# Kernel tuning notes

Measured on AMD Instinct MI355X. Metric: run time of the kernel, lower is better.

The kernel has to match this reference:

```python
import jax, jax.numpy as jnp
import numpy as np

DIM = 512; NH = 8; AG = 144; WIN = 18; PS = 12; B = 128; N0 = 320


def _pool_matrix(in_size, out_size):
    # PyTorch AdaptiveAvgPool2d window rule: start=floor(i*in/out), end=ceil((i+1)*in/out)
    P = np.zeros((out_size, in_size), np.float32)
    for i in range(out_size):
        s = (i * in_size) // out_size
        e = -((-(i + 1) * in_size) // out_size)
        P[i, s:e] = 1.0 / (e - s)
    return jnp.asarray(P)


def setup_inputs() -> dict:
    key = jax.random.key(0)
    ks = jax.random.split(key, 12)
    std = 0.02
    return {
        "x": jax.random.normal(ks[0], (B, N0, DIM), jnp.float32),
        "qkv_w": jax.random.normal(ks[1], (DIM, 3 * DIM), jnp.float32) * 0.02,
        "proj_w": jax.random.normal(ks[2], (DIM, DIM), jnp.float32) * 0.02,
        "proj_b": jnp.zeros((DIM,), jnp.float32),
        "dwc_w": jax.random.normal(ks[3], (DIM, 1, 3, 3), jnp.float32) * 0.1,
        "dwc_b": jnp.zeros((DIM,), jnp.float32),
        "an_bias": jax.random.normal(ks[4], (NH, AG, 7, 7), jnp.float32) * std,
        "na_bias": jax.random.normal(ks[5], (NH, AG, 7, 7), jnp.float32) * std,
        "ah_bias": jax.random.normal(ks[6], (1, NH, AG, WIN, 1), jnp.float32) * std,
        "aw_bias": jax.random.normal(ks[7], (1, NH, AG, 1, WIN), jnp.float32) * std,
        "ha_bias": jax.random.normal(ks[8], (1, NH, WIN, 1, AG), jnp.float32) * std,
        "wa_bias": jax.random.normal(ks[9], (1, NH, 1, WIN, AG), jnp.float32) * std,
    }


def reference(x, qkv_w, proj_w, proj_b, dwc_w, dwc_b,
              an_bias, na_bias, ah_bias, aw_bias, ha_bias, wa_bias):
    b, n0, c = x.shape
    x1 = jnp.pad(x, ((0, 0), (2, 2), (0, 0)))          # pad 2 tokens each side
    n = n0 + 4
    h = w = int(n ** 0.5)
    hd = c // NH
    scale = hd ** -0.5

    qkv = x1 @ qkv_w                                    # (b, n, 3c), no bias
    q, k, v = jnp.split(qkv, 3, axis=-1)

    # agent tokens: adaptive avg pool of q on the (h, w) grid to (PS, PS)
    P = _pool_matrix(h, PS)                             # (12, 18)
    qg = q.reshape(b, h, w, c)
    agent = jnp.einsum('oh,bhwc,pw->bopc', P, qg, P).reshape(b, AG, c)

    def heads(t):
        return t.reshape(b, n, NH, hd).transpose(0, 2, 1, 3)
    q, k, v = heads(q), heads(k), heads(v)              # (b, H, n, hd)
    ag = agent.reshape(b, AG, NH, hd).transpose(0, 2, 1, 3)  # (b, H, A, hd)

    # stage 1: agent <- keys  (ac_bias is concatenated then sliced off => no-op)
    pb1 = jax.image.resize(an_bias, (NH, AG, WIN, WIN), 'bilinear').reshape(1, NH, AG, WIN * WIN)
    pb2 = (ah_bias + aw_bias).reshape(1, NH, AG, WIN * WIN)
    agent_attn = jax.nn.softmax(
        jnp.einsum('bhad,bhnd->bhan', ag * scale, k) + pb1 + pb2, axis=-1)
    agent_v = jnp.einsum('bhan,bhnd->bhad', agent_attn, v)   # (b, H, A, hd)

    # stage 2: queries <- agents (ca_bias sliced off => no-op)
    ab1 = jax.image.resize(na_bias, (NH, AG, WIN, WIN), 'bilinear') \
        .reshape(1, NH, AG, WIN * WIN).transpose(0, 1, 3, 2)  # (1, H, n, A)
    ab2 = (ha_bias + wa_bias).reshape(1, NH, WIN * WIN, AG)
    q_attn = jax.nn.softmax(
        jnp.einsum('bhnd,bhad->bhna', q * scale, ag) + ab1 + ab2, axis=-1)
    out = jnp.einsum('bhna,bhad->bhnd', q_attn, agent_v)
    out = out.transpose(0, 2, 1, 3).reshape(b, n, c)

    # depthwise conv skip on v
    vimg = v.transpose(0, 2, 1, 3).reshape(b, h, w, c).transpose(0, 3, 1, 2)  # (b, c, h, w)
    dwc = jax.lax.conv_general_dilated(vimg, dwc_w, (1, 1), 'SAME',
                                       feature_group_count=c)
    dwc = dwc + dwc_b[None, :, None, None]
    out = out + dwc.transpose(0, 2, 3, 1).reshape(b, n, c)

    out = out @ proj_w + proj_b
    return out[:, 2:-2, :]
```

## Files before the change

kernel.cpp:

```cpp
#include <hip/hip_runtime.h>

typedef unsigned short u16;
typedef short bf16x8 __attribute__((ext_vector_type(8)));
typedef float f32x4 __attribute__((ext_vector_type(4)));

#define B_    128
#define N0_   320
#define C_    512
#define NH_   8
#define HD_   64
#define NTOK  324
#define H_    18
#define AG_   144
#define SCALE 0.125f

typedef __attribute__((address_space(3))) unsigned int as3_u32;
typedef __attribute__((address_space(1))) const unsigned int as1_u32;

__device__ __forceinline__ void gl_lds16(const void* g, void* l) {
  __builtin_amdgcn_global_load_lds((as1_u32*)(unsigned long long)g,
                                   (as3_u32*)(unsigned int)(unsigned long long)l,
                                   16, 0, 0);
}

__device__ __forceinline__ float bfu2f(u16 u) {
  union { unsigned int u; float f; } v; v.u = ((unsigned int)u) << 16; return v.f;
}
__device__ __forceinline__ u16 f2bfu(float f) {
  union { float f; unsigned int u; } v; v.f = f;
  unsigned int r = v.u + 0x7fffu + ((v.u >> 16) & 1u);
  return (u16)(r >> 16);
}

__global__ __launch_bounds__(256) void conv_x(const float* __restrict__ x, u16* __restrict__ xp)
{
  const int idx = blockIdx.x * 256 + threadIdx.x;
  const int row = idx >> 6, c8 = idx & 63;
  const int b = row / NTOK, t = row - b * NTOK;
  u16 o[8];
  if (t < 2 || t >= 322) {
    #pragma unroll
    for (int j = 0; j < 8; ++j) o[j] = 0;
  } else {
    const float* src = x + ((size_t)(b * N0_ + (t - 2))) * C_ + c8 * 8;
    const float4 f0 = *(const float4*)(src);
    const float4 f1 = *(const float4*)(src + 4);
    o[0]=f2bfu(f0.x); o[1]=f2bfu(f0.y); o[2]=f2bfu(f0.z); o[3]=f2bfu(f0.w);
    o[4]=f2bfu(f1.x); o[5]=f2bfu(f1.y); o[6]=f2bfu(f1.z); o[7]=f2bfu(f1.w);
  }
  *(bf16x8*)&xp[(size_t)row * C_ + c8 * 8] = *(bf16x8*)o;
}

__global__ __launch_bounds__(256) void tconv(const float* __restrict__ W, u16* __restrict__ Wt, int ncols)
{
  __shared__ float T[64][65];
  const int k0 = blockIdx.x * 64, n0 = blockIdx.y * 64;
  const int tid = threadIdx.x;
  const int rr = tid >> 4, cc = tid & 15;
  #pragma unroll
  for (int i = 0; i < 4; ++i) {
    const float4 f = *(const float4*)&W[(size_t)(k0 + i * 16 + rr) * ncols + n0 + cc * 4];
    T[i * 16 + rr][cc * 4 + 0] = f.x; T[i * 16 + rr][cc * 4 + 1] = f.y;
    T[i * 16 + rr][cc * 4 + 2] = f.z; T[i * 16 + rr][cc * 4 + 3] = f.w;
  }
  __syncthreads();
  #pragma unroll
  for (int i = 0; i < 4; ++i) {
    const int n = i * 16 + rr;
    ushort4 u;
    u.x = f2bfu(T[cc * 4 + 0][n]); u.y = f2bfu(T[cc * 4 + 1][n]);
    u.z = f2bfu(T[cc * 4 + 2][n]); u.w = f2bfu(T[cc * 4 + 3][n]);
    *(ushort4*)&Wt[(size_t)(n0 + n) * 512 + k0 + cc * 4] = u;
  }
}

template<int MODE>
__global__ __launch_bounds__(256) void mfma_gemm(
    const u16* __restrict__ A, const u16* __restrict__ Bt,
    u16* __restrict__ qb, u16* __restrict__ kb, u16* __restrict__ vb,
    const float* __restrict__ bias, float* __restrict__ outf)
{
  __shared__ __align__(16) u16 As[128 * 64];
  __shared__ __align__(16) u16 Bs[128 * 64];
  const int bx = blockIdx.x;
  const int by = blockIdx.y;
  const int tid = threadIdx.x;
  const int wv = tid >> 6, lane = tid & 63;
  const int lr = lane & 15, lk = lane >> 4;
  const int wr = wv >> 1, wc = wv & 1;
  const int si = lane >> 3, slot = lane & 7;

  size_t arow_src[4];
  #pragma unroll
  for (int jj = 0; jj < 4; ++jj) {
    const int rl = (wv * 4 + jj) * 8 + si;
    const int r = by * 128 + rl;
    if (MODE == 0) {
      arow_src[jj] = (size_t)r;
    } else {
      const int b2 = r / N0_, ii = r - b2 * N0_;
      arow_src[jj] = (size_t)b2 * NTOK + ii + 2;
    }
  }

  f32x4 acc[4][4] = {};
  for (int k0 = 0; k0 < 512; k0 += 64) {
    __syncthreads();
    #pragma unroll
    for (int jj = 0; jj < 4; ++jj) {
      const int rl = (wv * 4 + jj) * 8 + si;
      const int c = slot ^ (rl & 7);
      gl_lds16(A + arow_src[jj] * 512 + k0 + c * 8,
               (char*)As + (wv * 4 + jj) * 1024);
      gl_lds16(Bt + (size_t)(bx * 128 + rl) * 512 + k0 + c * 8,
               (char*)Bs + (wv * 4 + jj) * 1024);
    }
    __syncthreads();
    #pragma unroll
    for (int kk = 0; kk < 2; ++kk) {
      bf16x8 af[4], bf[4];
      #pragma unroll
      for (int m = 0; m < 4; ++m) {
        const int row = wr * 64 + m * 16 + lr;
        af[m] = *(const bf16x8*)((const char*)As + row * 128 + (((kk * 4 + lk) ^ (row & 7)) << 4));
      }
      #pragma unroll
      for (int n = 0; n < 4; ++n) {
        const int row = wc * 64 + n * 16 + lr;
        bf[n] = *(const bf16x8*)((const char*)Bs + row * 128 + (((kk * 4 + lk) ^ (row & 7)) << 4));
      }
      #pragma unroll
      for (int m = 0; m < 4; ++m)
        #pragma unroll
        for (int n = 0; n < 4; ++n)
          acc[m][n] = __builtin_amdgcn_mfma_f32_16x16x32_bf16(af[m], bf[n], acc[m][n], 0, 0, 0);
    }
  }

  if (MODE == 0) {
    const int mat = (bx * 128) >> 9;
    u16* outp = (mat == 0) ? qb : (mat == 1) ? kb : vb;
    #pragma unroll
    for (int m = 0; m < 4; ++m) {
      #pragma unroll
      for (int r = 0; r < 4; ++r) {
        const int row = by * 128 + wr * 64 + m * 16 + lk * 4 + r;
        const int b = row / NTOK, t = row - b * NTOK;
        #pragma unroll
        for (int n = 0; n < 4; ++n) {
          const int col = bx * 128 + wc * 64 + n * 16 + lr;
          const int rem = col & 511, h = rem >> 6, d = rem & 63;
          outp[(((size_t)(b * NH_ + h)) * NTOK + t) * HD_ + d] = f2bfu(acc[m][n][r]);
        }
      }
    }
  } else {
    #pragma unroll
    for (int m = 0; m < 4; ++m) {
      #pragma unroll
      for (int r = 0; r < 4; ++r) {
        const int row = by * 128 + wr * 64 + m * 16 + lk * 4 + r;
        #pragma unroll
        for (int n = 0; n < 4; ++n) {
          const int col = bx * 128 + wc * 64 + n * 16 + lr;
          outf[(size_t)row * C_ + col] = acc[m][n][r] + bias[col];
        }
      }
    }
  }
}

__global__ void bias_kernel(const float* __restrict__ an, const float* __restrict__ na,
                            const float* __restrict__ ah, const float* __restrict__ aw,
                            const float* __restrict__ ha, const float* __restrict__ wa,
                            float* __restrict__ bAN, float* __restrict__ bNA)
{
  const int blk = blockIdx.x;
  const int h = blk / AG_, a = blk - h * AG_;
  const int tid = threadIdx.x;
  if (tid >= NTOK) return;
  const int y = tid / H_, x = tid - y * H_;
  float cy = (y + 0.5f) * (7.0f / 18.0f) - 0.5f; cy = fminf(fmaxf(cy, 0.f), 6.f);
  float cx = (x + 0.5f) * (7.0f / 18.0f) - 0.5f; cx = fminf(fmaxf(cx, 0.f), 6.f);
  const int y0 = (int)floorf(cy); const float ty = cy - y0; const int y1 = min(y0 + 1, 6);
  const int x0 = (int)floorf(cx); const float tx = cx - x0; const int x1 = min(x0 + 1, 6);
  const float w00 = (1.f - ty) * (1.f - tx), w01 = (1.f - ty) * tx;
  const float w10 = ty * (1.f - tx), w11 = ty * tx;
  const float* anp = an + (size_t)blk * 49;
  const float* nap = na + (size_t)blk * 49;
  const float van = w00 * anp[y0*7+x0] + w01 * anp[y0*7+x1] + w10 * anp[y1*7+x0] + w11 * anp[y1*7+x1];
  const float vna = w00 * nap[y0*7+x0] + w01 * nap[y0*7+x1] + w10 * nap[y1*7+x0] + w11 * nap[y1*7+x1];
  bAN[(size_t)blk * NTOK + tid] = van + ah[(size_t)blk * H_ + y] + aw[(size_t)blk * H_ + x];
  bNA[((size_t)h * NTOK + tid) * AG_ + a] =
      vna + ha[((size_t)h * H_ + y) * AG_ + a] + wa[((size_t)h * H_ + x) * AG_ + a];
}

__global__ __launch_bounds__(512) void pool_kernel(const u16* __restrict__ qb, u16* __restrict__ agb)
{
  const int blk = blockIdx.x;
  const int b = blk / AG_, a = blk - b * AG_;
  const int o = a / 12, pc = a - o * 12;
  const int y0 = (3 * o) >> 1, x0 = (3 * pc) >> 1;
  const int c = threadIdx.x; const int h = c >> 6, d = c & 63;
  const size_t base = ((size_t)(b * NH_ + h)) * NTOK * HD_ + d;
  const int t00 = (y0 * H_ + x0) * HD_;
  const float v = bfu2f(qb[base + t00]) + bfu2f(qb[base + t00 + HD_])
                + bfu2f(qb[base + t00 + H_ * HD_]) + bfu2f(qb[base + t00 + H_ * HD_ + HD_]);
  agb[((size_t)(b * NH_ + h)) * AG_ * HD_ + a * HD_ + d] = f2bfu(0.25f * v);
}

__global__ __launch_bounds__(512) void dwc_kernel(
    const u16* __restrict__ vb, const float* __restrict__ dwc_w,
    const float* __restrict__ dwc_b, u16* __restrict__ aob)
{
  __shared__ __align__(16) u16 vL[NTOK * 64];
  const int bh = blockIdx.x, b = bh >> 3, h = bh & 7;
  const int tid = threadIdx.x;
  const bf16x8* vs = (const bf16x8*)(vb + (size_t)bh * NTOK * HD_);
  for (int idx = tid; idx < NTOK * 8; idx += 512)
    ((bf16x8*)vL)[idx] = vs[idx];
  const int d = tid & 63, tg = tid >> 6;
  float w9[9];
  #pragma unroll
  for (int j = 0; j < 9; ++j) w9[j] = dwc_w[(size_t)(h * 64 + d) * 9 + j];
  const float cb = dwc_b[h * 64 + d];
  __syncthreads();
  for (int t = tg; t < NTOK; t += 8) {
    const int y = t / H_, x = t - y * H_;
    float conv = cb;
    #pragma unroll
    for (int ky = 0; ky < 3; ++ky) {
      const int yy = y + ky - 1;
      if (yy < 0 || yy >= H_) continue;
      #pragma unroll
      for (int kx = 0; kx < 3; ++kx) {
        const int xc = x + kx - 1;
        if (xc < 0 || xc >= H_) continue;
        conv += w9[ky * 3 + kx] * bfu2f(vL[(yy * H_ + xc) * 64 + d]);
      }
    }
    aob[((size_t)b * NTOK + t) * C_ + h * 64 + d] = f2bfu(conv);
  }
}

__global__ __launch_bounds__(576) void stage1_v2(
    const u16* __restrict__ kb, const u16* __restrict__ vb,
    const u16* __restrict__ agb, const float* __restrict__ bAN,
    u16* __restrict__ avbT)
{
  __shared__ __align__(16) u16 vT[64 * 360];
  __shared__ __align__(16) u16 pW[9][16][40];
  const int bh = blockIdx.x, h = bh & 7;
  const int tid = threadIdx.x;

  for (int idx = tid; idx < 64 * 16; idx += 576)
    avbT[((size_t)bh * 64 + (idx >> 4)) * 160 + 144 + (idx & 15)] = 0;

  const u16* vsrc = vb + (size_t)bh * NTOK * HD_;
  for (int idx = tid; idx < 64 * 352; idx += 576) {
    const int d = idx & 63, n = idx >> 6;
    vT[d * 360 + n] = (n < NTOK) ? vsrc[n * HD_ + d] : (u16)0;
  }
  __syncthreads();

  const int mt = tid >> 6;
  const int l  = tid & 63, lr = l & 15, lk = l >> 4;

  const u16* aga = agb + ((size_t)bh * AG_ + mt * 16 + lr) * HD_ + lk * 8;
  const bf16x8 a0 = *(const bf16x8*)(aga);
  const bf16x8 a1 = *(const bf16x8*)(aga + 32);

  f32x4 acc[21];
  const u16* kbase = kb + (size_t)bh * NTOK * HD_ + lk * 8;
  #pragma unroll
  for (int nt = 0; nt < 21; ++nt) {
    const bf16x8 b0 = *(const bf16x8*)(kbase + (size_t)(nt * 16 + lr) * HD_);
    const bf16x8 b1 = *(const bf16x8*)(kbase + (size_t)(nt * 16 + lr) * HD_ + 32);
    f32x4 c = {0.f, 0.f, 0.f, 0.f};
    c = __builtin_amdgcn_mfma_f32_16x16x32_bf16(a0, b0, c, 0, 0, 0);
    c = __builtin_amdgcn_mfma_f32_16x16x32_bf16(a1, b1, c, 0, 0, 0);
    acc[nt] = c;
  }

  const float* bb = bAN + ((size_t)h * AG_ + mt * 16) * NTOK;
  float mx[4] = {-1e30f, -1e30f, -1e30f, -1e30f};
  #pragma unroll
  for (int nt = 0; nt < 21; ++nt) {
    const int col = nt * 16 + lr;
    const bool valid = (nt < 20) || (lr < 4);
    #pragma unroll
    for (int r = 0; r < 4; ++r) {
      float s = -1e30f;
      if (valid) s = acc[nt][r] * SCALE + bb[(lk * 4 + r) * NTOK + col];
      acc[nt][r] = s;
      mx[r] = fmaxf(mx[r], s);
    }
  }
  #pragma unroll
  for (int r = 0; r < 4; ++r) {
    #pragma unroll
    for (int o = 1; o < 16; o <<= 1) mx[r] = fmaxf(mx[r], __shfl_xor(mx[r], o));
  }
  float sm[4] = {0.f, 0.f, 0.f, 0.f};
  #pragma unroll
  for (int nt = 0; nt < 21; ++nt) {
    #pragma unroll
    for (int r = 0; r < 4; ++r) {
      const float e = __expf(acc[nt][r] - mx[r]);
      acc[nt][r] = e;
      sm[r] += e;
    }
  }
  #pragma unroll
  for (int r = 0; r < 4; ++r) {
    #pragma unroll
    for (int o = 1; o < 16; o <<= 1) sm[r] += __shfl_xor(sm[r], o);
    sm[r] = 1.0f / sm[r];
  }

  f32x4 ov[4];
  #pragma unroll
  for (int nt2 = 0; nt2 < 4; ++nt2) ov[nt2] = (f32x4){0.f, 0.f, 0.f, 0.f};
  for (int ks = 0; ks < 11; ++ks) {
    #pragma unroll
    for (int half = 0; half < 2; ++half) {
      const int nt = 2 * ks + half;
      #pragma unroll
      for (int r = 0; r < 4; ++r)
        pW[mt][lk * 4 + r][half * 16 + lr] = (nt < 21) ? f2bfu(acc[nt][r] * sm[r]) : (u16)0;
    }
    const bf16x8 pa = *(const bf16x8*)&pW[mt][lr][lk * 8];
    #pragma unroll
    for (int nt2 = 0; nt2 < 4; ++nt2) {
      const bf16x8 vf = *(const bf16x8*)&vT[(nt2 * 16 + lr) * 360 + ks * 32 + lk * 8];
      ov[nt2] = __builtin_amdgcn_mfma_f32_16x16x32_bf16(pa, vf, ov[nt2], 0, 0, 0);
    }
  }
  #pragma unroll
  for (int nt2 = 0; nt2 < 4; ++nt2) {
    #pragma unroll
    for (int r = 0; r < 4; ++r)
      avbT[((size_t)bh * 64 + nt2 * 16 + lr) * 160 + mt * 16 + lk * 4 + r] = f2bfu(ov[nt2][r]);
  }
}

__global__ __launch_bounds__(512) void stage2_v2(
    const u16* __restrict__ qb, const u16* __restrict__ agb,
    const u16* __restrict__ avbT, const float* __restrict__ bNA,
    u16* __restrict__ aob)
{
  __shared__ __align__(16) u16 pW[8][16][40];
  const int bh = blockIdx.x, b = bh >> 3, h = bh & 7;
  const int tid = threadIdx.x;
  const int wv = tid >> 6, l = tid & 63, lr = l & 15, lk = l >> 4;

  for (int mt = wv; mt < 21; mt += 8) {
    const int arow = min(mt * 16 + lr, NTOK - 1);
    const u16* qa = qb + ((size_t)bh * NTOK + arow) * HD_ + lk * 8;
    const bf16x8 a0 = *(const bf16x8*)(qa);
    const bf16x8 a1 = *(const bf16x8*)(qa + 32);

    f32x4 acc[9];
    #pragma unroll
    for (int nt = 0; nt < 9; ++nt) {
      const u16* bp = agb + ((size_t)bh * AG_ + nt * 16 + lr) * HD_ + lk * 8;
      f32x4 c = {0.f, 0.f, 0.f, 0.f};
      c = __builtin_amdgcn_mfma_f32_16x16x32_bf16(a0, *(const bf16x8*)(bp), c, 0, 0, 0);
      c = __builtin_amdgcn_mfma_f32_16x16x32_bf16(a1, *(const bf16x8*)(bp + 32), c, 0, 0, 0);
      acc[nt] = c;
    }

    float mx[4] = {-1e30f, -1e30f, -1e30f, -1e30f};
    #pragma unroll
    for (int nt = 0; nt < 9; ++nt) {
      #pragma unroll
      for (int r = 0; r < 4; ++r) {
        const int trow = min(mt * 16 + lk * 4 + r, NTOK - 1);
        const float s = acc[nt][r] * SCALE + bNA[((size_t)h * NTOK + trow) * AG_ + nt * 16 + lr];
        acc[nt][r] = s;
        mx[r] = fmaxf(mx[r], s);
      }
    }
    #pragma unroll
    for (int r = 0; r < 4; ++r) {
      #pragma unroll
      for (int o = 1; o < 16; o <<= 1) mx[r] = fmaxf(mx[r], __shfl_xor(mx[r], o));
    }
    float sm[4] = {0.f, 0.f, 0.f, 0.f};
    #pragma unroll
    for (int nt = 0; nt < 9; ++nt) {
      #pragma unroll
      for (int r = 0; r < 4; ++r) {
        const float e = __expf(acc[nt][r] - mx[r]);
        acc[nt][r] = e;
        sm[r] += e;
      }
    }
    #pragma unroll
    for (int r = 0; r < 4; ++r) {
      #pragma unroll
      for (int o = 1; o < 16; o <<= 1) sm[r] += __shfl_xor(sm[r], o);
      sm[r] = 1.0f / sm[r];
    }

    f32x4 ov[4];
    #pragma unroll
    for (int nt2 = 0; nt2 < 4; ++nt2) ov[nt2] = (f32x4){0.f, 0.f, 0.f, 0.f};
    const u16* avbase = avbT + (size_t)bh * 64 * 160;
    for (int ks = 0; ks < 5; ++ks) {
      #pragma unroll
      for (int half = 0; half < 2; ++half) {
        const int nt = 2 * ks + half;
        #pragma unroll
        for (int r = 0; r < 4; ++r)
          pW[wv][lk * 4 + r][half * 16 + lr] = (nt < 9) ? f2bfu(acc[nt][r] * sm[r]) : (u16)0;
      }
      const bf16x8 pa = *(const bf16x8*)&pW[wv][lr][lk * 8];
      #pragma unroll
      for (int nt2 = 0; nt2 < 4; ++nt2) {
        const bf16x8 vf = *(const bf16x8*)(avbase + (size_t)(nt2 * 16 + lr) * 160 + ks * 32 + lk * 8);
        ov[nt2] = __builtin_amdgcn_mfma_f32_16x16x32_bf16(pa, vf, ov[nt2], 0, 0, 0);
      }
    }

    #pragma unroll
    for (int nt2 = 0; nt2 < 4; ++nt2) {
      #pragma unroll
      for (int r = 0; r < 4; ++r) {
        const int t = mt * 16 + lk * 4 + r;
        if (t < NTOK) {
          const size_t o = ((size_t)b * NTOK + t) * C_ + h * 64 + nt2 * 16 + lr;
          aob[o] = f2bfu(bfu2f(aob[o]) + ov[nt2][r]);
        }
      }
    }
  }
}

extern "C" void kernel_launch(void* const* d_in, const int* in_sizes, int n_in,
                              void* d_out, int out_size, void* d_ws, size_t ws_size,
                              hipStream_t stream)
{
  (void)in_sizes; (void)n_in; (void)out_size;
  const float* x      = (const float*)d_in[0];
  const float* qkv_w  = (const float*)d_in[1];
  const float* proj_w = (const float*)d_in[2];
  const float* proj_b = (const float*)d_in[3];
  const float* dwc_w  = (const float*)d_in[4];
  const float* dwc_b  = (const float*)d_in[5];
  const float* an     = (const float*)d_in[6];
  const float* na     = (const float*)d_in[7];
  const float* ah     = (const float*)d_in[8];
  const float* aw     = (const float*)d_in[9];
  const float* ha     = (const float*)d_in[10];
  const float* wa     = (const float*)d_in[11];

  char* ws = (char*)d_ws;
  const size_t QB   = (size_t)B_ * NH_ * NTOK * HD_ * 2;
  const size_t AGB  = (size_t)B_ * NH_ * AG_  * HD_ * 2;
  const size_t AVTB = (size_t)B_ * NH_ * 64 * 160 * 2;
  const size_t BB   = (size_t)NH_ * AG_ * NTOK * 4;
  const size_t WQ   = (size_t)1536 * 512 * 2;
  const size_t WP   = (size_t)512 * 512 * 2;
  u16* qb    = (u16*)(ws);
  u16* kb    = (u16*)(ws + QB);
  u16* vb    = (u16*)(ws + 2 * QB);
  u16* xp    = (u16*)(ws + 3 * QB);
  u16* agb   = (u16*)(ws + 3 * QB);
  u16* avbT  = (u16*)(ws + 3 * QB + AGB);
  float* bAN = (float*)(ws + 3 * QB + AGB + AVTB);
  u16* wqkvT = (u16*)(ws + 4 * QB);
  u16* wprojT= (u16*)(ws + 4 * QB + WQ);
  float* bNA = (float*)(ws + 4 * QB + WQ + WP);
  u16* aob   = kb;
  if (ws_size < 4 * QB + WQ + WP + BB) return;

  conv_x   <<<dim3(B_ * NTOK * 64 / 256), dim3(256), 0, stream>>>(x, xp);
  tconv    <<<dim3(8, 24), dim3(256), 0, stream>>>(qkv_w, wqkvT, 1536);
  tconv    <<<dim3(8, 8),  dim3(256), 0, stream>>>(proj_w, wprojT, 512);
  mfma_gemm<0><<<dim3(12, 324), dim3(256), 0, stream>>>(xp, wqkvT, qb, kb, vb, nullptr, nullptr);
  pool_kernel<<<dim3(B_ * AG_),  dim3(512), 0, stream>>>(qb, agb);
  bias_kernel<<<dim3(NH_ * AG_), dim3(324), 0, stream>>>(an, na, ah, aw, ha, wa, bAN, bNA);
  stage1_v2<<<dim3(B_ * NH_),  dim3(576), 0, stream>>>(kb, vb, agb, bAN, avbT);
  dwc_kernel<<<dim3(B_ * NH_), dim3(512), 0, stream>>>(vb, dwc_w, dwc_b, aob);
  stage2_v2<<<dim3(B_ * NH_),  dim3(512), 0, stream>>>(qb, agb, avbT, bNA, aob);
  mfma_gemm<1><<<dim3(4, 320), dim3(256), 0, stream>>>(aob, wprojT, nullptr, nullptr, nullptr, proj_b, (float*)d_out);
}
```

Before: 482.6 us.

## Fuse agent-attention stages and depthwise conv into one kernel with head-major output

Merges stage1, the depthwise-conv kernel and stage2 into a single per-(batch,head) kernel. Agent values stay in LDS instead of going through a global scratch buffer, and the conv reads the already transposed V tile from LDS. The output is written head-major, so the projection GEMM's A-load addressing now gathers per head chunk. This removes two launches and several global round trips (avbT, and the read-modify-write of aob). The cost is more LDS per block and a serial stage2 loop spread over 9 waves.

Result: slower. 526.8 us (+9.2%).

```diff
diff --git a/kernel.cpp b/kernel.cpp
--- a/kernel.cpp
+++ b/kernel.cpp
@@ -96,10 +96,10 @@
     const int rl = (wv * 4 + jj) * 8 + si;
     const int r = by * 128 + rl;
     if (MODE == 0) {
-      arow_src[jj] = (size_t)r;
+      arow_src[jj] = (size_t)r * 512;
     } else {
       const int b2 = r / N0_, ii = r - b2 * N0_;
-      arow_src[jj] = (size_t)b2 * NTOK + ii + 2;
+      arow_src[jj] = ((size_t)b2 * 8 * NTOK + (ii + 2)) * 64;
     }
   }
 
@@ -110,8 +110,10 @@
     for (int jj = 0; jj < 4; ++jj) {
       const int rl = (wv * 4 + jj) * 8 + si;
       const int c = slot ^ (rl & 7);
-      gl_lds16(A + arow_src[jj] * 512 + k0 + c * 8,
-               (char*)As + (wv * 4 + jj) * 1024);
+      const u16* asrc = (MODE == 0)
+          ? (A + arow_src[jj] + k0 + c * 8)
+          : (A + arow_src[jj] + (size_t)(k0 >> 6) * (NTOK * 64) + c * 8);
+      gl_lds16(asrc, (char*)As + (wv * 4 + jj) * 1024);
       gl_lds16(Bt + (size_t)(bx * 128 + rl) * 512 + k0 + c * 8,
                (char*)Bs + (wv * 4 + jj) * 1024);
     }
@@ -209,62 +211,35 @@
   agb[((size_t)(b * NH_ + h)) * AG_ * HD_ + a * HD_ + d] = f2bfu(0.25f * v);
 }
 
-__global__ __launch_bounds__(512) void dwc_kernel(
-    const u16* __restrict__ vb, const float* __restrict__ dwc_w,
-    const float* __restrict__ dwc_b, u16* __restrict__ aob)
-{
-  __shared__ __align__(16) u16 vL[NTOK * 64];
-  const int bh = blockIdx.x, b = bh >> 3, h = bh & 7;
-  const int tid = threadIdx.x;
-  const bf16x8* vs = (const bf16x8*)(vb + (size_t)bh * NTOK * HD_);
-  for (int idx = tid; idx < NTOK * 8; idx += 512)
-    ((bf16x8*)vL)[idx] = vs[idx];
-  const int d = tid & 63, tg = tid >> 6;
-  float w9[9];
-  #pragma unroll
-  for (int j = 0; j < 9; ++j) w9[j] = dwc_w[(size_t)(h * 64 + d) * 9 + j];
-  const float cb = dwc_b[h * 64 + d];
-  __syncthreads();
-  for (int t = tg; t < NTOK; t += 8) {
-    const int y = t / H_, x = t - y * H_;
-    float conv = cb;
-    #pragma unroll
-    for (int ky = 0; ky < 3; ++ky) {
-      const int yy = y + ky - 1;
-      if (yy < 0 || yy >= H_) continue;
-      #pragma unroll
-      for (int kx = 0; kx < 3; ++kx) {
-        const int xc = x + kx - 1;
-        if (xc < 0 || xc >= H_) continue;
-        conv += w9[ky * 3 + kx] * bfu2f(vL[(yy * H_ + xc) * 64 + d]);
-      }
-    }
-    aob[((size_t)b * NTOK + t) * C_ + h * 64 + d] = f2bfu(conv);
-  }
-}
-
-__global__ __launch_bounds__(576) void stage1_v2(
+__global__ __launch_bounds__(576) void fused_attn(
     const u16* __restrict__ kb, const u16* __restrict__ vb,
-    const u16* __restrict__ agb, const float* __restrict__ bAN,
-    u16* __restrict__ avbT)
+    const u16* __restrict__ qb, const u16* __restrict__ agb,
+    const float* __restrict__ bAN, const float* __restrict__ bNA,
+    const float* __restrict__ dwc_w, const float* __restrict__ dwc_b,
+    u16* __restrict__ aob)
 {
   __shared__ __align__(16) u16 vT[64 * 360];
+  __shared__ __align__(16) u16 avT[64 * 168];
   __shared__ __align__(16) u16 pW[9][16][40];
   const int bh = blockIdx.x, h = bh & 7;
   const int tid = threadIdx.x;
-
-  for (int idx = tid; idx < 64 * 16; idx += 576)
-    avbT[((size_t)bh * 64 + (idx >> 4)) * 160 + 144 + (idx & 15)] = 0;
+  const int mt = tid >> 6;
+  const int l = tid & 63, lr = l & 15, lk = l >> 4;
+
+  for (int idx = tid; idx < 128; idx += 576)
+    *(bf16x8*)&avT[(idx >> 1) * 168 + 144 + (idx & 1) * 8] = (bf16x8){0,0,0,0,0,0,0,0};
 
   const u16* vsrc = vb + (size_t)bh * NTOK * HD_;
-  for (int idx = tid; idx < 64 * 352; idx += 576) {
-    const int d = idx & 63, n = idx >> 6;
-    vT[d * 360 + n] = (n < NTOK) ? vsrc[n * HD_ + d] : (u16)0;
-  }
-  __syncthreads();
-
-  const int mt = tid >> 6;
-  const int l  = tid & 63, lr = l & 15, lk = l >> 4;
+  for (int idx = tid; idx < 64 * 45; idx += 576) {
+    const int d = idx & 63, c = idx >> 6;
+    bf16x8 tv;
+    #pragma unroll
+    for (int j = 0; j < 8; ++j) {
+      const int n = c * 8 + j;
+      tv[j] = (n < NTOK) ? (short)vsrc[(size_t)n * HD_ + d] : (short)0;
+    }
+    *(bf16x8*)&vT[d * 360 + c * 8] = tv;
+  }
 
   const u16* aga = agb + ((size_t)bh * AG_ + mt * 16 + lr) * HD_ + lk * 8;
   const bf16x8 a0 = *(const bf16x8*)(aga);
@@ -318,6 +293,8 @@
     sm[r] = 1.0f / sm[r];
   }
 
+  __syncthreads();
+
   f32x4 ov[4];
   #pragma unroll
   for (int nt2 = 0; nt2 < 4; ++nt2) ov[nt2] = (f32x4){0.f, 0.f, 0.f, 0.f};
@@ -338,99 +315,109 @@
   }
   #pragma unroll
   for (int nt2 = 0; nt2 < 4; ++nt2) {
-    #pragma unroll
-    for (int r = 0; r < 4; ++r)
-      avbT[((size_t)bh * 64 + nt2 * 16 + lr) * 160 + mt * 16 + lk * 4 + r] = f2bfu(ov[nt2][r]);
-  }
-}
-
-__global__ __launch_bounds__(512) void stage2_v2(
-    const u16* __restrict__ qb, const u16* __restrict__ agb,
-    const u16* __restrict__ avbT, const float* __restrict__ bNA,
-    u16* __restrict__ aob)
-{
-  __shared__ __align__(16) u16 pW[8][16][40];
-  const int bh = blockIdx.x, b = bh >> 3, h = bh & 7;
-  const int tid = threadIdx.x;
-  const int wv = tid >> 6, l = tid & 63, lr = l & 15, lk = l >> 4;
-
-  for (int mt = wv; mt < 21; mt += 8) {
-    const int arow = min(mt * 16 + lr, NTOK - 1);
+    ushort4 u;
+    u.x = f2bfu(ov[nt2][0]); u.y = f2bfu(ov[nt2][1]);
+    u.z = f2bfu(ov[nt2][2]); u.w = f2bfu(ov[nt2][3]);
+    *(ushort4*)&avT[(nt2 * 16 + lr) * 168 + mt * 16 + lk * 4] = u;
+  }
+
+  __syncthreads();
+
+  u16* aout = aob + (size_t)bh * NTOK * HD_;
+  for (int mt2 = mt; mt2 < 21; mt2 += 9) {
+    const int arow = min(mt2 * 16 + lr, NTOK - 1);
     const u16* qa = qb + ((size_t)bh * NTOK + arow) * HD_ + lk * 8;
-    const bf16x8 a0 = *(const bf16x8*)(qa);
-    const bf16x8 a1 = *(const bf16x8*)(qa + 32);
-
-    f32x4 acc[9];
+    const bf16x8 qa0 = *(const bf16x8*)(qa);
+    const bf16x8 qa1 = *(const bf16x8*)(qa + 32);
+
+    f32x4 acc2[9];
     #pragma unroll
     for (int nt = 0; nt < 9; ++nt) {
       const u16* bp = agb + ((size_t)bh * AG_ + nt * 16 + lr) * HD_ + lk * 8;
       f32x4 c = {0.f, 0.f, 0.f, 0.f};
-      c = __builtin_amdgcn_mfma_f32_16x16x32_bf16(a0, *(const bf16x8*)(bp), c, 0, 0, 0);
-      c = __builtin_amdgcn_mfma_f32_16x16x32_bf16(a1, *(const bf16x8*)(bp + 32), c, 0, 0, 0);
-      acc[nt] = c;
-    }
-
-    float mx[4] = {-1e30f, -1e30f, -1e30f, -1e30f};
+      c = __builtin_amdgcn_mfma_f32_16x16x32_bf16(qa0, *(const bf16x8*)(bp), c, 0, 0, 0);
+      c = __builtin_amdgcn_mfma_f32_16x16x32_bf16(qa1, *(const bf16x8*)(bp + 32), c, 0, 0, 0);
+      acc2[nt] = c;
+    }
+
+    float mx2[4] = {-1e30f, -1e30f, -1e30f, -1e30f};
     #pragma unroll
     for (int nt = 0; nt < 9; ++nt) {
       #pragma unroll
       for (int r = 0; r < 4; ++r) {
-        const int trow = min(mt * 16 + lk * 4 + r, NTOK - 1);
-        const float s = acc[nt][r] * SCALE + bNA[((size_t)h * NTOK + trow) * AG_ + nt * 16 + lr];
-        acc[nt][r] = s;
-        mx[r] = fmaxf(mx[r], s);
+        const int trow = min(mt2 * 16 + lk * 4 + r, NTOK - 1);
+        const float s = acc2[nt][r] * SCALE + bNA[((size_t)h * NTOK + trow) * AG_ + nt * 16 + lr];
+        acc2[nt][r] = s;
+        mx2[r] = fmaxf(mx2[r], s);
       }
     }
     #pragma unroll
     for (int r = 0; r < 4; ++r) {
       #pragma unroll
-      for (int o = 1; o < 16; o <<= 1) mx[r] = fmaxf(mx[r], __shfl_xor(mx[r], o));
-    }
-    float sm[4] = {0.f, 0.f, 0.f, 0.f};
+      for (int o = 1; o < 16; o <<= 1) mx2[r] = fmaxf(mx2[r], __shfl_xor(mx2[r], o));
+    }
+    float sm2[4] = {0.f, 0.f, 0.f, 0.f};
     #pragma unroll
     for (int nt = 0; nt < 9; ++nt) {
       #pragma unroll
       for (int r = 0; r < 4; ++r) {
-        const float e = __expf(acc[nt][r] - mx[r]);
-        acc[nt][r] = e;
-        sm[r] += e;
+        const float e = __expf(acc2[nt][r] - mx2[r]);
+        acc2[nt][r] = e;
+        sm2[r] += e;
       }
     }
     #pragma unroll
     for (int r = 0; r < 4; ++r) {
       #pragma unroll
-      for (int o = 1; o < 16; o <<= 1) sm[r] += __shfl_xor(sm[r], o);
-      sm[r] = 1.0f / sm[r];
-    }
-
-    f32x4 ov[4];
-    #pragma unroll
-    for (int nt2 = 0; nt2 < 4; ++nt2) ov[nt2] = (f32x4){0.f, 0.f, 0.f, 0.f};
-    const u16* avbase = avbT + (size_t)bh * 64 * 160;
+      for (int o = 1; o < 16; o <<= 1) sm2[r] += __shfl_xor(sm2[r], o);
+      sm2[r] = 1.0f / sm2[r];
+    }
+
+    f32x4 ov2[4];
+    #pragma unroll
+    for (int nt2 = 0; nt2 < 4; ++nt2) ov2[nt2] = (f32x4){0.f, 0.f, 0.f, 0.f};
     for (int ks = 0; ks < 5; ++ks) {
       #pragma unroll
       for (int half = 0; half < 2; ++half) {
         const int nt = 2 * ks + half;
         #pragma unroll
         for (int r = 0; r < 4; ++r)
-          pW[wv][lk * 4 + r][half * 16 + lr] = (nt < 9) ? f2bfu(acc[nt][r] * sm[r]) : (u16)0;
-      }
-      const bf16x8 pa = *(const bf16x8*)&pW[wv][lr][lk * 8];
+          pW[mt][lk * 4 + r][half * 16 + lr] = (nt < 9) ? f2bfu(acc2[nt][r] * sm2[r]) : (u16)0;
+      }
+      const bf16x8 pa = *(const bf16x8*)&pW[mt][lr][lk * 8];
       #pragma unroll
       for (int nt2 = 0; nt2 < 4; ++nt2) {
-        const bf16x8 vf = *(const bf16x8*)(avbase + (size_t)(nt2 * 16 + lr) * 160 + ks * 32 + lk * 8);
-        ov[nt2] = __builtin_amdgcn_mfma_f32_16x16x32_bf16(pa, vf, ov[nt2], 0, 0, 0);
+        const bf16x8 vf = *(const bf16x8*)&avT[(nt2 * 16 + lr) * 168 + ks * 32 + lk * 8];
+        ov2[nt2] = __builtin_amdgcn_mfma_f32_16x16x32_bf16(pa, vf, ov2[nt2], 0, 0, 0);
       }
     }
 
     #pragma unroll
     for (int nt2 = 0; nt2 < 4; ++nt2) {
+      const int d = nt2 * 16 + lr;
+      const float* wp = dwc_w + (size_t)(h * 64 + d) * 9;
+      float w9[9];
+      #pragma unroll
+      for (int j = 0; j < 9; ++j) w9[j] = wp[j];
+      const float cb = dwc_b[h * 64 + d];
       #pragma unroll
       for (int r = 0; r < 4; ++r) {
-        const int t = mt * 16 + lk * 4 + r;
+        const int t = mt2 * 16 + lk * 4 + r;
         if (t < NTOK) {
-          const size_t o = ((size_t)b * NTOK + t) * C_ + h * 64 + nt2 * 16 + lr;
-          aob[o] = f2bfu(bfu2f(aob[o]) + ov[nt2][r]);
+          const int y = t / H_, x = t - y * H_;
+          float conv = cb;
+          #pragma unroll
+          for (int ky = 0; ky < 3; ++ky) {
+            const int yy = y + ky - 1;
+            if (yy < 0 || yy >= H_) continue;
+            #pragma unroll
+            for (int kx = 0; kx < 3; ++kx) {
+              const int xc = x + kx - 1;
+              if (xc < 0 || xc >= H_) continue;
+              conv += w9[ky * 3 + kx] * bfu2f(vT[d * 360 + yy * H_ + xc]);
+            }
+          }
+          aout[(size_t)t * HD_ + d] = f2bfu(ov2[nt2][r] + conv);
         }
       }
     }
@@ -456,24 +443,22 @@
   const float* wa     = (const float*)d_in[11];
 
   char* ws = (char*)d_ws;
-  const size_t QB   = (size_t)B_ * NH_ * NTOK * HD_ * 2;
-  const size_t AGB  = (size_t)B_ * NH_ * AG_  * HD_ * 2;
-  const size_t AVTB = (size_t)B_ * NH_ * 64 * 160 * 2;
-  const size_t BB   = (size_t)NH_ * AG_ * NTOK * 4;
-  const size_t WQ   = (size_t)1536 * 512 * 2;
-  const size_t WP   = (size_t)512 * 512 * 2;
+  const size_t QB  = (size_t)B_ * NH_ * NTOK * HD_ * 2;
+  const size_t AGB = (size_t)B_ * NH_ * AG_  * HD_ * 2;
+  const size_t BB  = (size_t)NH_ * AG_ * NTOK * 4;
+  const size_t WQ  = (size_t)1536 * 512 * 2;
+  const size_t WP  = (size_t)512 * 512 * 2;
   u16* qb    = (u16*)(ws);
   u16* kb    = (u16*)(ws + QB);
   u16* vb    = (u16*)(ws + 2 * QB);
   u16* xp    = (u16*)(ws + 3 * QB);
   u16* agb   = (u16*)(ws + 3 * QB);
-  u16* avbT  = (u16*)(ws + 3 * QB + AGB);
-  float* bAN = (float*)(ws + 3 * QB + AGB + AVTB);
+  float* bAN = (float*)(ws + 3 * QB + AGB);
+  float* bNA = (float*)(ws + 3 * QB + AGB + BB);
   u16* wqkvT = (u16*)(ws + 4 * QB);
   u16* wprojT= (u16*)(ws + 4 * QB + WQ);
-  float* bNA = (float*)(ws + 4 * QB + WQ + WP);
   u16* aob   = kb;
-  if (ws_size < 4 * QB + WQ + WP + BB) return;
+  if (ws_size < 4 * QB + WQ + WP) return;
 
   conv_x   <<<dim3(B_ * NTOK * 64 / 256), dim3(256), 0, stream>>>(x, xp);
   tconv    <<<dim3(8, 24), dim3(256), 0, stream>>>(qkv_w, wqkvT, 1536);
@@ -481,8 +466,6 @@
   mfma_gemm<0><<<dim3(12, 324), dim3(256), 0, stream>>>(xp, wqkvT, qb, kb, vb, nullptr, nullptr);
   pool_kernel<<<dim3(B_ * AG_),  dim3(512), 0, stream>>>(qb, agb);
   bias_kernel<<<dim3(NH_ * AG_), dim3(324), 0, stream>>>(an, na, ah, aw, ha, wa, bAN, bNA);
-  stage1_v2<<<dim3(B_ * NH_),  dim3(576), 0, stream>>>(kb, vb, agb, bAN, avbT);
-  dwc_kernel<<<dim3(B_ * NH_), dim3(512), 0, stream>>>(vb, dwc_w, dwc_b, aob);
-  stage2_v2<<<dim3(B_ * NH_),  dim3(512), 0, stream>>>(qb, agb, avbT, bNA, aob);
+  fused_attn<<<dim3(B_ * NH_), dim3(576), 0, stream>>>(kb, vb, qb, agb, bAN, bNA, dwc_w, dwc_b, aob);
   mfma_gemm<1><<<dim3(4, 320), dim3(256), 0, stream>>>(aob, wprojT, nullptr, nullptr, nullptr, proj_b, (float*)d_out);
 }
```
